# Kernel optimization log

Hardware: AMD Instinct MI355X
Metric: run time of the kernel (lower is better)

## Reference

```python
import jax, jax.numpy as jnp
from jax import lax
import numpy as np

E, D, I, T, K = 32, 1024, 512, 4096, 8

def setup_inputs() -> dict:
    key = jax.random.key(0)
    k1, k2, k3, k4, k5 = jax.random.split(key, 5)
    hidden_states = jax.random.normal(k1, (T, D), dtype=jnp.float32)
    top_k_indices = jax.random.randint(k2, (T, K), 0, E, dtype=jnp.int64)
    w = jax.random.uniform(k3, (T, K), dtype=jnp.float32)
    top_k_weights = w / jnp.sum(w, axis=-1, keepdims=True)  # normalised routing weights
    gate_up_proj = jax.random.normal(k4, (E, 2 * I, D), dtype=jnp.float32) * 0.05
    down_proj = jax.random.normal(k5, (E, D, I), dtype=jnp.float32) * 0.05
    return {
        'hidden_states': hidden_states,
        'top_k_indices': top_k_indices,
        'top_k_weights': top_k_weights,
        'gate_up_proj': gate_up_proj,
        'down_proj': down_proj,
    }


def _moe(hidden_states, top_k_indices, top_k_weights, gate_up_proj, down_proj):
    num_experts = gate_up_proj.shape[0]
    # combine[t, e] = sum over k-slots routed to expert e of top_k_weights[t, k].
    # Duplicate expert ids in a token's top-k sum their weights, matching the
    # torch loop which index_add's each (k, tok) pair separately (outputs identical).
    onehot = jax.nn.one_hot(top_k_indices, num_experts, dtype=hidden_states.dtype)  # [T,K,E]
    combine = jnp.einsum('tke,tk->te', onehot, top_k_weights)  # [T,E]

    def body(acc, ew):
        W_gu, W_d, c = ew  # [2I,D], [D,I], [T]
        gu = hidden_states @ W_gu.T  # [T,2I]
        gate, up = jnp.split(gu, 2, axis=-1)
        h = jax.nn.silu(gate) * up  # SwiGLU
        y = h @ W_d.T  # [T,D]
        return acc + c[:, None] * y, None

    out, _ = lax.scan(body, jnp.zeros_like(hidden_states),
                      (gate_up_proj, down_proj, combine.T))
    return out


def reference(hidden_states, top_k_indices, top_k_weights, gate_up_proj, down_proj):
    return _moe(hidden_states, top_k_indices, top_k_weights, gate_up_proj, down_proj)
```

## Files before the change

### kernel.cpp

```cpp
#include <hip/hip_runtime.h>
#include <hip/hip_bf16.h>

#define E_   32
#define D_   1024
#define I_   512
#define T_   4096
#define KTOP 8
#define TK   (T_*KTOP)

#define BM   128
#define BKK  32
#define PAD  40
#define MAXT (TK/BM + E_)

#define TILES_OFF 1024
#define TOK_OFF   8192
#define WT_OFF    139264
#define H_OFF     524288

typedef __attribute__((ext_vector_type(8))) short short8v;
typedef __attribute__((ext_vector_type(4))) float f32x4;

__device__ inline unsigned short f2bf(float x) {
    __hip_bfloat16 h = __float2bfloat16(x);
    union { __hip_bfloat16 h; unsigned short u; } c; c.h = h; return c.u;
}
__device__ inline short8v pack8(float4 a, float4 b) {
    short8v r;
    r[0]=(short)f2bf(a.x); r[1]=(short)f2bf(a.y); r[2]=(short)f2bf(a.z); r[3]=(short)f2bf(a.w);
    r[4]=(short)f2bf(b.x); r[5]=(short)f2bf(b.y); r[6]=(short)f2bf(b.z); r[7]=(short)f2bf(b.w);
    return r;
}


__global__ void detect_idx64_kernel(const int* __restrict__ idx32, int* w) {
    const int lane = threadIdx.x;
    int bad = 0;
#pragma unroll
    for (int j = 0; j < 4; ++j) bad |= idx32[2 * (lane + 64 * j) + 1];
    int allz = __all(bad == 0);
    if (lane == 0) w[0] = allz ? 1 : 0;
}

__global__ void count_kernel(const int* __restrict__ idx32, int* w) {
    int i = blockIdx.x * blockDim.x + threadIdx.x;
    if (i >= TK) return;
    int e = w[0] ? idx32[2*i] : idx32[i];
    atomicAdd(&w[32 + e], 1);
}

__global__ void scan_kernel(int* w) {
    const int lane = threadIdx.x;
    int cnt = (lane < E_) ? w[32 + lane] : 0;
    int x = cnt;
#pragma unroll
    for (int d = 1; d < 32; d <<= 1) {
        int v = __shfl_up(x, d, 64);
        if (lane >= d) x += v;
    }
    int excl = x - cnt;
    if (lane < E_) w[96 + lane] = excl;
    if (lane == E_ - 1) w[96 + E_] = x;

    int nt_e = (lane < E_) ? (cnt + BM - 1) / BM : 0;
    int y = nt_e;
#pragma unroll
    for (int d = 1; d < 32; d <<= 1) {
        int v = __shfl_up(y, d, 64);
        if (lane >= d) y += v;
    }
    int texcl = y - nt_e;
    if (lane == E_ - 1) w[129] = y;
    int2* tiles = (int2*)((char*)w + TILES_OFF);
    for (int i = 0; i < nt_e; ++i)
        tiles[texcl + i] = make_int2(lane, excl + i * BM);
}

__global__ void scatter_kernel(const int* __restrict__ idx32,
                               const float* __restrict__ wts, int* w) {
    int i = blockIdx.x * blockDim.x + threadIdx.x;
    if (i >= TK) return;
    int e = w[0] ? idx32[2*i] : idx32[i];
    int p = atomicAdd(&w[64 + e], 1);
    int pos = w[96 + e] + p;
    ((int*)  ((char*)w + TOK_OFF))[pos] = i / KTOP;
    ((float*)((char*)w + WT_OFF))[pos]  = wts[i];
}

__global__ __launch_bounds__(256) void gemm1_mfma(
    const float* __restrict__ hidden, const float* __restrict__ gup,
    const int* __restrict__ w, unsigned short* __restrict__ H)
{
    if ((int)blockIdx.y >= w[129]) return;
    int2 tl = ((const int2*)((const char*)w + TILES_OFF))[blockIdx.y];
    const int e = tl.x, rs = tl.y;
    const int rows = min(w[96 + e + 1] - rs, BM);
    const int* tok = (const int*)((const char*)w + TOK_OFF);

    __shared__ short As[BM * PAD];
    __shared__ short Bs[BM * PAD];
    __shared__ int tokS[BM];

    const int tid = threadIdx.x;
    if (tid < BM) tokS[tid] = tok[rs + min(tid, rows - 1)];
    __syncthreads();

    const int n0 = blockIdx.x * 64;
    const float* gb = gup + (size_t)e * (2 * I_) * D_;

    const int crow = tid >> 2, ckg = tid & 3;
    const float* aptr0 = hidden + (size_t)tokS[crow]      * D_ + ckg * 8;
    const float* aptr1 = hidden + (size_t)tokS[crow + 64] * D_ + ckg * 8;
    const float* bptr0 = gb + (size_t)(n0 + crow)      * D_ + ckg * 8;
    const float* bptr1 = gb + (size_t)(I_ + n0 + crow) * D_ + ckg * 8;
    short8v* wA0 = (short8v*)&As[crow * PAD + ckg * 8];
    short8v* wA1 = (short8v*)&As[(crow + 64) * PAD + ckg * 8];
    short8v* wB0 = (short8v*)&Bs[crow * PAD + ckg * 8];
    short8v* wB1 = (short8v*)&Bs[(crow + 64) * PAD + ckg * 8];

    const int wid = tid >> 6, lane = tid & 63;
    const int l16 = lane & 15, lk = (lane >> 4) * 8;
    const int aoff = (wid * 32 + l16) * PAD + lk;
    const int boff = l16 * PAD + lk;

    f32x4 acc[2][8];
#pragma unroll
    for (int i = 0; i < 2; ++i)
#pragma unroll
        for (int j = 0; j < 8; ++j) acc[i][j] = (f32x4){0.f, 0.f, 0.f, 0.f};

    float4 ra0a, ra0b, ra1a, ra1b, rb0a, rb0b, rb1a, rb1b;
#define LOADREGS1(K0) { \
    ra0a = *(const float4*)(aptr0 + (K0)); ra0b = *(const float4*)(aptr0 + (K0) + 4); \
    ra1a = *(const float4*)(aptr1 + (K0)); ra1b = *(const float4*)(aptr1 + (K0) + 4); \
    rb0a = *(const float4*)(bptr0 + (K0)); rb0b = *(const float4*)(bptr0 + (K0) + 4); \
    rb1a = *(const float4*)(bptr1 + (K0)); rb1b = *(const float4*)(bptr1 + (K0) + 4); }

    LOADREGS1(0);
    for (int k0 = 0; k0 < D_; k0 += BKK) {
        __syncthreads();
        *wA0 = pack8(ra0a, ra0b);
        *wA1 = pack8(ra1a, ra1b);
        *wB0 = pack8(rb0a, rb0b);
        *wB1 = pack8(rb1a, rb1b);
        __syncthreads();
        if (k0 + BKK < D_) LOADREGS1(k0 + BKK);
        short8v a0 = *(const short8v*)&As[aoff];
        short8v a1 = *(const short8v*)&As[aoff + 16 * PAD];
#pragma unroll
        for (int j = 0; j < 8; ++j) {
            short8v b = *(const short8v*)&Bs[boff + j * 16 * PAD];
            acc[0][j] = __builtin_amdgcn_mfma_f32_16x16x32_bf16(a0, b, acc[0][j], 0, 0, 0);
            acc[1][j] = __builtin_amdgcn_mfma_f32_16x16x32_bf16(a1, b, acc[1][j], 0, 0, 0);
        }
    }

    const int r0 = (lane >> 4) * 4;
#pragma unroll
    for (int mr = 0; mr < 2; ++mr)
#pragma unroll
        for (int j = 0; j < 4; ++j)
#pragma unroll
            for (int r = 0; r < 4; ++r) {
                int m = wid * 32 + mr * 16 + r0 + r;
                if (m < rows) {
                    float g = acc[mr][j][r], u = acc[mr][j + 4][r];
                    float s = g / (1.f + __expf(-g));
                    H[(size_t)(rs + m) * I_ + n0 + j * 16 + l16] = f2bf(s * u);
                }
            }
}

__global__ __launch_bounds__(256) void gemm2_mfma(
    const unsigned short* __restrict__ H, const float* __restrict__ down,
    const int* __restrict__ w, float* __restrict__ out)
{
    if ((int)blockIdx.y >= w[129]) return;
    int2 tl = ((const int2*)((const char*)w + TILES_OFF))[blockIdx.y];
    const int e = tl.x, rs = tl.y;
    const int rows = min(w[96 + e + 1] - rs, BM);
    const int*   tok = (const int*)  ((const char*)w + TOK_OFF);
    const float* wts = (const float*)((const char*)w + WT_OFF);

    __shared__ short As[BM * PAD];
    __shared__ short Bs[BM * PAD];
    __shared__ int   tokS[BM];
    __shared__ float wtS[BM];

    const int tid = threadIdx.x;
    if (tid < BM) {
        tokS[tid] = tok[rs + min(tid, rows - 1)];
        wtS[tid]  = (tid < rows) ? wts[rs + tid] : 0.f;
    }
    __syncthreads();

    const int n0 = blockIdx.x * 128;
    const float* db = down + (size_t)e * D_ * I_;

    const int crow = tid >> 2, ckg = tid & 3;
    const short* ha0 = (const short*)H + (size_t)min(rs + crow,      TK - 1) * I_ + ckg * 8;
    const short* ha1 = (const short*)H + (size_t)min(rs + crow + 64, TK - 1) * I_ + ckg * 8;
    const float* bptr0 = db + (size_t)(n0 + crow)      * I_ + ckg * 8;
    const float* bptr1 = db + (size_t)(n0 + crow + 64) * I_ + ckg * 8;
    short8v* wA0 = (short8v*)&As[crow * PAD + ckg * 8];
    short8v* wA1 = (short8v*)&As[(crow + 64) * PAD + ckg * 8];
    short8v* wB0 = (short8v*)&Bs[crow * PAD + ckg * 8];
    short8v* wB1 = (short8v*)&Bs[(crow + 64) * PAD + ckg * 8];

    const int wid = tid >> 6, lane = tid & 63;
    const int l16 = lane & 15, lk = (lane >> 4) * 8;
    const int aoff = (wid * 32 + l16) * PAD + lk;
    const int boff = l16 * PAD + lk;

    f32x4 acc[2][8];
#pragma unroll
    for (int i = 0; i < 2; ++i)
#pragma unroll
        for (int j = 0; j < 8; ++j) acc[i][j] = (f32x4){0.f, 0.f, 0.f, 0.f};

    short8v raa, rab;
    float4 rb0a, rb0b, rb1a, rb1b;
#define LOADREGS2(K0) { \
    raa = *(const short8v*)(ha0 + (K0)); rab = *(const short8v*)(ha1 + (K0)); \
    rb0a = *(const float4*)(bptr0 + (K0)); rb0b = *(const float4*)(bptr0 + (K0) + 4); \
    rb1a = *(const float4*)(bptr1 + (K0)); rb1b = *(const float4*)(bptr1 + (K0) + 4); }

    LOADREGS2(0);
    for (int k0 = 0; k0 < I_; k0 += BKK) {
        __syncthreads();
        *wA0 = raa;
        *wA1 = rab;
        *wB0 = pack8(rb0a, rb0b);
        *wB1 = pack8(rb1a, rb1b);
        __syncthreads();
        if (k0 + BKK < I_) LOADREGS2(k0 + BKK);
        short8v a0 = *(const short8v*)&As[aoff];
        short8v a1 = *(const short8v*)&As[aoff + 16 * PAD];
#pragma unroll
        for (int j = 0; j < 8; ++j) {
            short8v b = *(const short8v*)&Bs[boff + j * 16 * PAD];
            acc[0][j] = __builtin_amdgcn_mfma_f32_16x16x32_bf16(a0, b, acc[0][j], 0, 0, 0);
            acc[1][j] = __builtin_amdgcn_mfma_f32_16x16x32_bf16(a1, b, acc[1][j], 0, 0, 0);
        }
    }

    const int r0 = (lane >> 4) * 4;
#pragma unroll
    for (int mr = 0; mr < 2; ++mr)
#pragma unroll
        for (int j = 0; j < 8; ++j)
#pragma unroll
            for (int r = 0; r < 4; ++r) {
                int m = wid * 32 + mr * 16 + r0 + r;
                if (m < rows)
                    atomicAdd(&out[(size_t)tokS[m] * D_ + n0 + j * 16 + l16],
                              wtS[m] * acc[mr][j][r]);
            }
}


extern "C" void kernel_launch(void* const* d_in, const int* in_sizes, int n_in,
                              void* d_out, int out_size, void* d_ws, size_t ws_size,
                              hipStream_t stream)
{
    const float* hidden = (const float*)d_in[0];
    const int*   idx    = (const int*)  d_in[1];
    const float* wts    = (const float*)d_in[2];
    const float* gup    = (const float*)d_in[3];
    const float* down   = (const float*)d_in[4];
    float* out = (float*)d_out;
    int*   w   = (int*)d_ws;

    hipMemsetAsync(d_ws, 0, 8192, stream);
    hipMemsetAsync(d_out, 0, (size_t)T_ * D_ * sizeof(float), stream);

    detect_idx64_kernel<<<1, 64, 0, stream>>>(idx, w);
    count_kernel<<<(TK + 255) / 256, 256, 0, stream>>>(idx, w);
    scan_kernel<<<1, 64, 0, stream>>>(w);
    scatter_kernel<<<(TK + 255) / 256, 256, 0, stream>>>(idx, wts, w);

    unsigned short* H = (unsigned short*)((char*)d_ws + H_OFF);
    dim3 g1(I_ / 64, MAXT), g2(D_ / 128, MAXT);
    gemm1_mfma<<<g1, 256, 0, stream>>>(hidden, gup, w, H);
    gemm2_mfma<<<g2, 256, 0, stream>>>(H, down, w, out);
}
```

Before: 687.4 us.

## Use k-octet-major LDS layout and per-block histogram routing with local atomics

The shared-memory tiles move from a padded row-major layout to a k-octet-major layout, [oct][row][8]. Each thread now loads one row across two k-octets, and each MFMA fragment read is a contiguous 16-byte slot, which is meant to reduce LDS bank conflicts and simplify addressing. Routing replaces global atomics with per-block shared-memory histograms and per-block base offsets computed in a serial scan, so contention on global counters goes away. The scan kernel now does a serial loop over 128 blocks per expert, and the global load pattern changes (strided 16-float gaps per thread), which may affect coalescing.

Result: slower. 705.5 us (+2.6%).

```diff
diff --git a/kernel.cpp b/kernel.cpp
--- a/kernel.cpp
+++ b/kernel.cpp
@@ -10,12 +10,14 @@
 
 #define BM   128
 #define BKK  32
-#define PAD  40
 #define MAXT (TK/BM + E_)
+#define NBLK 128
 
 #define TILES_OFF 1024
-#define TOK_OFF   8192
-#define WT_OFF    139264
+#define HIST_OFF  4096
+#define BASE_OFF  20480
+#define TOK_OFF   36864
+#define WT_OFF    167936
 #define H_OFF     524288
 
 typedef __attribute__((ext_vector_type(8))) short short8v;
@@ -42,16 +44,26 @@
     if (lane == 0) w[0] = allz ? 1 : 0;
 }
 
-__global__ void count_kernel(const int* __restrict__ idx32, int* w) {
-    int i = blockIdx.x * blockDim.x + threadIdx.x;
-    if (i >= TK) return;
+__global__ __launch_bounds__(256) void hist_kernel(const int* __restrict__ idx32, int* w) {
+    __shared__ int h[E_];
+    const int tid = threadIdx.x, b = blockIdx.x;
+    if (tid < E_) h[tid] = 0;
+    __syncthreads();
+    int i = b * 256 + tid;
     int e = w[0] ? idx32[2*i] : idx32[i];
-    atomicAdd(&w[32 + e], 1);
+    atomicAdd(&h[e], 1);
+    __syncthreads();
+    if (tid < E_) ((int*)((char*)w + HIST_OFF))[b * E_ + tid] = h[tid];
 }
 
 __global__ void scan_kernel(int* w) {
     const int lane = threadIdx.x;
-    int cnt = (lane < E_) ? w[32 + lane] : 0;
+    int* hist = (int*)((char*)w + HIST_OFF);
+    int* base = (int*)((char*)w + BASE_OFF);
+    int cnt = 0;
+    if (lane < E_) {
+        for (int b = 0; b < NBLK; ++b) { base[b*E_ + lane] = cnt; cnt += hist[b*E_ + lane]; }
+    }
     int x = cnt;
 #pragma unroll
     for (int d = 1; d < 32; d <<= 1) {
@@ -59,7 +71,10 @@
         if (lane >= d) x += v;
     }
     int excl = x - cnt;
-    if (lane < E_) w[96 + lane] = excl;
+    if (lane < E_) {
+        w[96 + lane] = excl;
+        for (int b = 0; b < NBLK; ++b) base[b*E_ + lane] += excl;
+    }
     if (lane == E_ - 1) w[96 + E_] = x;
 
     int nt_e = (lane < E_) ? (cnt + BM - 1) / BM : 0;
@@ -76,14 +91,16 @@
         tiles[texcl + i] = make_int2(lane, excl + i * BM);
 }
 
-__global__ void scatter_kernel(const int* __restrict__ idx32,
+__global__ __launch_bounds__(256) void scatter_kernel(const int* __restrict__ idx32,
                                const float* __restrict__ wts, int* w) {
-    int i = blockIdx.x * blockDim.x + threadIdx.x;
-    if (i >= TK) return;
+    __shared__ int cur[E_];
+    const int tid = threadIdx.x, b = blockIdx.x;
+    if (tid < E_) cur[tid] = ((int*)((char*)w + BASE_OFF))[b * E_ + tid];
+    __syncthreads();
+    int i = b * 256 + tid;
     int e = w[0] ? idx32[2*i] : idx32[i];
-    int p = atomicAdd(&w[64 + e], 1);
-    int pos = w[96 + e] + p;
-    ((int*)  ((char*)w + TOK_OFF))[pos] = i / KTOP;
+    int pos = atomicAdd(&cur[e], 1);
+    ((int*)  ((char*)w + TOK_OFF))[pos] = i >> 3;
     ((float*)((char*)w + WT_OFF))[pos]  = wts[i];
 }
 
@@ -97,8 +114,8 @@
     const int rows = min(w[96 + e + 1] - rs, BM);
     const int* tok = (const int*)((const char*)w + TOK_OFF);
 
-    __shared__ short As[BM * PAD];
-    __shared__ short Bs[BM * PAD];
+    __shared__ short As[4 * BM * 8];
+    __shared__ short Bs[4 * BM * 8];
     __shared__ int tokS[BM];
 
     const int tid = threadIdx.x;
@@ -108,20 +125,19 @@
     const int n0 = blockIdx.x * 64;
     const float* gb = gup + (size_t)e * (2 * I_) * D_;
 
-    const int crow = tid >> 2, ckg = tid & 3;
-    const float* aptr0 = hidden + (size_t)tokS[crow]      * D_ + ckg * 8;
-    const float* aptr1 = hidden + (size_t)tokS[crow + 64] * D_ + ckg * 8;
-    const float* bptr0 = gb + (size_t)(n0 + crow)      * D_ + ckg * 8;
-    const float* bptr1 = gb + (size_t)(I_ + n0 + crow) * D_ + ckg * 8;
-    short8v* wA0 = (short8v*)&As[crow * PAD + ckg * 8];
-    short8v* wA1 = (short8v*)&As[(crow + 64) * PAD + ckg * 8];
-    short8v* wB0 = (short8v*)&Bs[crow * PAD + ckg * 8];
-    short8v* wB1 = (short8v*)&Bs[(crow + 64) * PAD + ckg * 8];
+    const int srow = tid & 127, oct0 = tid >> 7;
+    const float* asrc = hidden + (size_t)tokS[srow] * D_ + oct0 * 8;
+    const float* bsrc = (srow < 64 ? gb + (size_t)(n0 + srow) * D_
+                                   : gb + (size_t)(I_ + n0 + srow - 64) * D_) + oct0 * 8;
+    short8v* wA0 = (short8v*)&As[(oct0 * BM + srow) * 8];
+    short8v* wA1 = (short8v*)&As[((oct0 + 2) * BM + srow) * 8];
+    short8v* wB0 = (short8v*)&Bs[(oct0 * BM + srow) * 8];
+    short8v* wB1 = (short8v*)&Bs[((oct0 + 2) * BM + srow) * 8];
 
     const int wid = tid >> 6, lane = tid & 63;
-    const int l16 = lane & 15, lk = (lane >> 4) * 8;
-    const int aoff = (wid * 32 + l16) * PAD + lk;
-    const int boff = l16 * PAD + lk;
+    const int l16 = lane & 15, koct = lane >> 4;
+    const int aoff = koct * BM + wid * 32 + l16;
+    const int boff = koct * BM + l16;
 
     f32x4 acc[2][8];
 #pragma unroll
@@ -129,27 +145,27 @@
 #pragma unroll
         for (int j = 0; j < 8; ++j) acc[i][j] = (f32x4){0.f, 0.f, 0.f, 0.f};
 
-    float4 ra0a, ra0b, ra1a, ra1b, rb0a, rb0b, rb1a, rb1b;
+    float4 ra0, ra1, ra2, ra3, rb0, rb1, rb2, rb3;
 #define LOADREGS1(K0) { \
-    ra0a = *(const float4*)(aptr0 + (K0)); ra0b = *(const float4*)(aptr0 + (K0) + 4); \
-    ra1a = *(const float4*)(aptr1 + (K0)); ra1b = *(const float4*)(aptr1 + (K0) + 4); \
-    rb0a = *(const float4*)(bptr0 + (K0)); rb0b = *(const float4*)(bptr0 + (K0) + 4); \
-    rb1a = *(const float4*)(bptr1 + (K0)); rb1b = *(const float4*)(bptr1 + (K0) + 4); }
+    ra0 = *(const float4*)(asrc + (K0));      ra1 = *(const float4*)(asrc + (K0) + 4); \
+    ra2 = *(const float4*)(asrc + (K0) + 16); ra3 = *(const float4*)(asrc + (K0) + 20); \
+    rb0 = *(const float4*)(bsrc + (K0));      rb1 = *(const float4*)(bsrc + (K0) + 4); \
+    rb2 = *(const float4*)(bsrc + (K0) + 16); rb3 = *(const float4*)(bsrc + (K0) + 20); }
 
     LOADREGS1(0);
     for (int k0 = 0; k0 < D_; k0 += BKK) {
         __syncthreads();
-        *wA0 = pack8(ra0a, ra0b);
-        *wA1 = pack8(ra1a, ra1b);
-        *wB0 = pack8(rb0a, rb0b);
-        *wB1 = pack8(rb1a, rb1b);
+        *wA0 = pack8(ra0, ra1);
+        *wA1 = pack8(ra2, ra3);
+        *wB0 = pack8(rb0, rb1);
+        *wB1 = pack8(rb2, rb3);
         __syncthreads();
         if (k0 + BKK < D_) LOADREGS1(k0 + BKK);
-        short8v a0 = *(const short8v*)&As[aoff];
-        short8v a1 = *(const short8v*)&As[aoff + 16 * PAD];
+        short8v a0 = *(const short8v*)&As[aoff * 8];
+        short8v a1 = *(const short8v*)&As[(aoff + 16) * 8];
 #pragma unroll
         for (int j = 0; j < 8; ++j) {
-            short8v b = *(const short8v*)&Bs[boff + j * 16 * PAD];
+            short8v b = *(const short8v*)&Bs[(boff + j * 16) * 8];
             acc[0][j] = __builtin_amdgcn_mfma_f32_16x16x32_bf16(a0, b, acc[0][j], 0, 0, 0);
             acc[1][j] = __builtin_amdgcn_mfma_f32_16x16x32_bf16(a1, b, acc[1][j], 0, 0, 0);
         }
@@ -182,8 +198,8 @@
     const int*   tok = (const int*)  ((const char*)w + TOK_OFF);
     const float* wts = (const float*)((const char*)w + WT_OFF);
 
-    __shared__ short As[BM * PAD];
-    __shared__ short Bs[BM * PAD];
+    __shared__ short As[4 * BM * 8];
+    __shared__ short Bs[4 * BM * 8];
     __shared__ int   tokS[BM];
     __shared__ float wtS[BM];
 
@@ -197,20 +213,18 @@
     const int n0 = blockIdx.x * 128;
     const float* db = down + (size_t)e * D_ * I_;
 
-    const int crow = tid >> 2, ckg = tid & 3;
-    const short* ha0 = (const short*)H + (size_t)min(rs + crow,      TK - 1) * I_ + ckg * 8;
-    const short* ha1 = (const short*)H + (size_t)min(rs + crow + 64, TK - 1) * I_ + ckg * 8;
-    const float* bptr0 = db + (size_t)(n0 + crow)      * I_ + ckg * 8;
-    const float* bptr1 = db + (size_t)(n0 + crow + 64) * I_ + ckg * 8;
-    short8v* wA0 = (short8v*)&As[crow * PAD + ckg * 8];
-    short8v* wA1 = (short8v*)&As[(crow + 64) * PAD + ckg * 8];
-    short8v* wB0 = (short8v*)&Bs[crow * PAD + ckg * 8];
-    short8v* wB1 = (short8v*)&Bs[(crow + 64) * PAD + ckg * 8];
+    const int srow = tid & 127, oct0 = tid >> 7;
+    const short* hsrc = (const short*)H + (size_t)min(rs + srow, TK - 1) * I_ + oct0 * 8;
+    const float* bsrc = db + (size_t)(n0 + srow) * I_ + oct0 * 8;
+    short8v* wA0 = (short8v*)&As[(oct0 * BM + srow) * 8];
+    short8v* wA1 = (short8v*)&As[((oct0 + 2) * BM + srow) * 8];
+    short8v* wB0 = (short8v*)&Bs[(oct0 * BM + srow) * 8];
+    short8v* wB1 = (short8v*)&Bs[((oct0 + 2) * BM + srow) * 8];
 
     const int wid = tid >> 6, lane = tid & 63;
-    const int l16 = lane & 15, lk = (lane >> 4) * 8;
-    const int aoff = (wid * 32 + l16) * PAD + lk;
-    const int boff = l16 * PAD + lk;
+    const int l16 = lane & 15, koct = lane >> 4;
+    const int aoff = koct * BM + wid * 32 + l16;
+    const int boff = koct * BM + l16;
 
     f32x4 acc[2][8];
 #pragma unroll
@@ -219,26 +233,26 @@
         for (int j = 0; j < 8; ++j) acc[i][j] = (f32x4){0.f, 0.f, 0.f, 0.f};
 
     short8v raa, rab;
-    float4 rb0a, rb0b, rb1a, rb1b;
+    float4 rb0, rb1, rb2, rb3;
 #define LOADREGS2(K0) { \
-    raa = *(const short8v*)(ha0 + (K0)); rab = *(const short8v*)(ha1 + (K0)); \
-    rb0a = *(const float4*)(bptr0 + (K0)); rb0b = *(const float4*)(bptr0 + (K0) + 4); \
-    rb1a = *(const float4*)(bptr1 + (K0)); rb1b = *(const float4*)(bptr1 + (K0) + 4); }
+    raa = *(const short8v*)(hsrc + (K0)); rab = *(const short8v*)(hsrc + (K0) + 16); \
+    rb0 = *(const float4*)(bsrc + (K0));      rb1 = *(const float4*)(bsrc + (K0) + 4); \
+    rb2 = *(const float4*)(bsrc + (K0) + 16); rb3 = *(const float4*)(bsrc + (K0) + 20); }
 
     LOADREGS2(0);
     for (int k0 = 0; k0 < I_; k0 += BKK) {
         __syncthreads();
         *wA0 = raa;
         *wA1 = rab;
-        *wB0 = pack8(rb0a, rb0b);
-        *wB1 = pack8(rb1a, rb1b);
+        *wB0 = pack8(rb0, rb1);
+        *wB1 = pack8(rb2, rb3);
         __syncthreads();
         if (k0 + BKK < I_) LOADREGS2(k0 + BKK);
-        short8v a0 = *(const short8v*)&As[aoff];
-        short8v a1 = *(const short8v*)&As[aoff + 16 * PAD];
+        short8v a0 = *(const short8v*)&As[aoff * 8];
+        short8v a1 = *(const short8v*)&As[(aoff + 16) * 8];
 #pragma unroll
         for (int j = 0; j < 8; ++j) {
-            short8v b = *(const short8v*)&Bs[boff + j * 16 * PAD];
+            short8v b = *(const short8v*)&Bs[(boff + j * 16) * 8];
             acc[0][j] = __builtin_amdgcn_mfma_f32_16x16x32_bf16(a0, b, acc[0][j], 0, 0, 0);
             acc[1][j] = __builtin_amdgcn_mfma_f32_16x16x32_bf16(a1, b, acc[1][j], 0, 0, 0);
         }
@@ -271,13 +285,13 @@
     float* out = (float*)d_out;
     int*   w   = (int*)d_ws;
 
-    hipMemsetAsync(d_ws, 0, 8192, stream);
+    hipMemsetAsync(d_ws, 0, 4096, stream);
     hipMemsetAsync(d_out, 0, (size_t)T_ * D_ * sizeof(float), stream);
 
     detect_idx64_kernel<<<1, 64, 0, stream>>>(idx, w);
-    count_kernel<<<(TK + 255) / 256, 256, 0, stream>>>(idx, w);
+    hist_kernel<<<NBLK, 256, 0, stream>>>(idx, w);
     scan_kernel<<<1, 64, 0, stream>>>(w);
-    scatter_kernel<<<(TK + 255) / 256, 256, 0, stream>>>(idx, wts, w);
+    scatter_kernel<<<NBLK, 256, 0, stream>>>(idx, wts, w);
 
     unsigned short* H = (unsigned short*)((char*)d_ws + H_OFF);
     dim3 g1(I_ / 64, MAXT), g2(D_ / 128, MAXT);
```

## Remap GEMM blocks for XCD-local L2 reuse and use per-block routing histograms

Applied to the files above, without the earlier changes.

The flat GEMM grid index is remapped so that all column blocks of a row tile go to the same XCD, with tiles split into contiguous chunks per XCD. This is meant to improve L2 reuse of the gathered hidden rows and the expert weights. Global-atomic counting and scatter are replaced by per-block shared-memory histograms with precomputed bases, which also gives a deterministic token order within each expert. The LDS row pad also changes from 40 to 36 shorts. That leaves 16-byte vector LDS accesses only 8-byte aligned, which may hurt throughput or correctness.

Result: faster. 626.3 us (-8.9%).

```diff
diff --git a/kernel.cpp b/kernel.cpp
--- a/kernel.cpp
+++ b/kernel.cpp
@@ -10,12 +10,16 @@
 
 #define BM   128
 #define BKK  32
-#define PAD  40
+#define PAD  36
 #define MAXT (TK/BM + E_)
+#define TCHUNK (MAXT/8)
+#define NBLK 128
 
 #define TILES_OFF 1024
-#define TOK_OFF   8192
-#define WT_OFF    139264
+#define HIST_OFF  4096
+#define BASE_OFF  20480
+#define TOK_OFF   36864
+#define WT_OFF    167936
 #define H_OFF     524288
 
 typedef __attribute__((ext_vector_type(8))) short short8v;
@@ -42,16 +46,26 @@
     if (lane == 0) w[0] = allz ? 1 : 0;
 }
 
-__global__ void count_kernel(const int* __restrict__ idx32, int* w) {
-    int i = blockIdx.x * blockDim.x + threadIdx.x;
-    if (i >= TK) return;
+__global__ __launch_bounds__(256) void hist_kernel(const int* __restrict__ idx32, int* w) {
+    __shared__ int h[E_];
+    const int tid = threadIdx.x, b = blockIdx.x;
+    if (tid < E_) h[tid] = 0;
+    __syncthreads();
+    int i = b * 256 + tid;
     int e = w[0] ? idx32[2*i] : idx32[i];
-    atomicAdd(&w[32 + e], 1);
+    atomicAdd(&h[e], 1);
+    __syncthreads();
+    if (tid < E_) ((int*)((char*)w + HIST_OFF))[b * E_ + tid] = h[tid];
 }
 
 __global__ void scan_kernel(int* w) {
     const int lane = threadIdx.x;
-    int cnt = (lane < E_) ? w[32 + lane] : 0;
+    int* hist = (int*)((char*)w + HIST_OFF);
+    int* base = (int*)((char*)w + BASE_OFF);
+    int cnt = 0;
+    if (lane < E_) {
+        for (int b = 0; b < NBLK; ++b) { base[b*E_ + lane] = cnt; cnt += hist[b*E_ + lane]; }
+    }
     int x = cnt;
 #pragma unroll
     for (int d = 1; d < 32; d <<= 1) {
@@ -59,7 +73,10 @@
         if (lane >= d) x += v;
     }
     int excl = x - cnt;
-    if (lane < E_) w[96 + lane] = excl;
+    if (lane < E_) {
+        w[96 + lane] = excl;
+        for (int b = 0; b < NBLK; ++b) base[b*E_ + lane] += excl;
+    }
     if (lane == E_ - 1) w[96 + E_] = x;
 
     int nt_e = (lane < E_) ? (cnt + BM - 1) / BM : 0;
@@ -76,14 +93,16 @@
         tiles[texcl + i] = make_int2(lane, excl + i * BM);
 }
 
-__global__ void scatter_kernel(const int* __restrict__ idx32,
+__global__ __launch_bounds__(256) void scatter_kernel(const int* __restrict__ idx32,
                                const float* __restrict__ wts, int* w) {
-    int i = blockIdx.x * blockDim.x + threadIdx.x;
-    if (i >= TK) return;
+    __shared__ int cur[E_];
+    const int tid = threadIdx.x, b = blockIdx.x;
+    if (tid < E_) cur[tid] = ((int*)((char*)w + BASE_OFF))[b * E_ + tid];
+    __syncthreads();
+    int i = b * 256 + tid;
     int e = w[0] ? idx32[2*i] : idx32[i];
-    int p = atomicAdd(&w[64 + e], 1);
-    int pos = w[96 + e] + p;
-    ((int*)  ((char*)w + TOK_OFF))[pos] = i / KTOP;
+    int pos = atomicAdd(&cur[e], 1);
+    ((int*)  ((char*)w + TOK_OFF))[pos] = i >> 3;
     ((float*)((char*)w + WT_OFF))[pos]  = wts[i];
 }
 
@@ -91,8 +110,11 @@
     const float* __restrict__ hidden, const float* __restrict__ gup,
     const int* __restrict__ w, unsigned short* __restrict__ H)
 {
-    if ((int)blockIdx.y >= w[129]) return;
-    int2 tl = ((const int2*)((const char*)w + TILES_OFF))[blockIdx.y];
+    const int s = blockIdx.y * 8 + blockIdx.x;
+    const int tile = (s & 7) * TCHUNK + (s >> 6);
+    const int cb   = (s >> 3) & 7;
+    if (tile >= w[129]) return;
+    int2 tl = ((const int2*)((const char*)w + TILES_OFF))[tile];
     const int e = tl.x, rs = tl.y;
     const int rows = min(w[96 + e + 1] - rs, BM);
     const int* tok = (const int*)((const char*)w + TOK_OFF);
@@ -105,7 +127,7 @@
     if (tid < BM) tokS[tid] = tok[rs + min(tid, rows - 1)];
     __syncthreads();
 
-    const int n0 = blockIdx.x * 64;
+    const int n0 = cb * 64;
     const float* gb = gup + (size_t)e * (2 * I_) * D_;
 
     const int crow = tid >> 2, ckg = tid & 3;
@@ -165,8 +187,8 @@
                 int m = wid * 32 + mr * 16 + r0 + r;
                 if (m < rows) {
                     float g = acc[mr][j][r], u = acc[mr][j + 4][r];
-                    float s = g / (1.f + __expf(-g));
-                    H[(size_t)(rs + m) * I_ + n0 + j * 16 + l16] = f2bf(s * u);
+                    float sgl = g / (1.f + __expf(-g));
+                    H[(size_t)(rs + m) * I_ + n0 + j * 16 + l16] = f2bf(sgl * u);
                 }
             }
 }
@@ -175,8 +197,11 @@
     const unsigned short* __restrict__ H, const float* __restrict__ down,
     const int* __restrict__ w, float* __restrict__ out)
 {
-    if ((int)blockIdx.y >= w[129]) return;
-    int2 tl = ((const int2*)((const char*)w + TILES_OFF))[blockIdx.y];
+    const int s = blockIdx.y * 8 + blockIdx.x;
+    const int tile = (s & 7) * TCHUNK + (s >> 6);
+    const int cb   = (s >> 3) & 7;
+    if (tile >= w[129]) return;
+    int2 tl = ((const int2*)((const char*)w + TILES_OFF))[tile];
     const int e = tl.x, rs = tl.y;
     const int rows = min(w[96 + e + 1] - rs, BM);
     const int*   tok = (const int*)  ((const char*)w + TOK_OFF);
@@ -194,7 +219,7 @@
     }
     __syncthreads();
 
-    const int n0 = blockIdx.x * 128;
+    const int n0 = cb * 128;
     const float* db = down + (size_t)e * D_ * I_;
 
     const int crow = tid >> 2, ckg = tid & 3;
@@ -271,16 +296,16 @@
     float* out = (float*)d_out;
     int*   w   = (int*)d_ws;
 
-    hipMemsetAsync(d_ws, 0, 8192, stream);
+    hipMemsetAsync(d_ws, 0, 4096, stream);
     hipMemsetAsync(d_out, 0, (size_t)T_ * D_ * sizeof(float), stream);
 
     detect_idx64_kernel<<<1, 64, 0, stream>>>(idx, w);
-    count_kernel<<<(TK + 255) / 256, 256, 0, stream>>>(idx, w);
+    hist_kernel<<<NBLK, 256, 0, stream>>>(idx, w);
     scan_kernel<<<1, 64, 0, stream>>>(w);
-    scatter_kernel<<<(TK + 255) / 256, 256, 0, stream>>>(idx, wts, w);
+    scatter_kernel<<<NBLK, 256, 0, stream>>>(idx, wts, w);
 
     unsigned short* H = (unsigned short*)((char*)d_ws + H_OFF);
-    dim3 g1(I_ / 64, MAXT), g2(D_ / 128, MAXT);
+    dim3 g1(8, MAXT), g2(8, MAXT);
     gemm1_mfma<<<g1, 256, 0, stream>>>(hidden, gup, w, H);
     gemm2_mfma<<<g2, 256, 0, stream>>>(H, down, w, out);
 }
```
